# Optimization experiments

Hardware: AMD Instinct MI355X
Metric: run time of the kernel (lower is better)

The kernel has to match this reference:

```python
import jax, jax.numpy as jnp
import numpy as np

N_EMBD = 384
HEAD_SIZE = 64
B, T = 512, 256


def setup_inputs() -> dict:
    key = jax.random.key(0)
    ks = jax.random.split(key, 7)
    s = 1.0 / np.sqrt(N_EMBD)  # torch Linear default init scale
    return {
        "x": jax.random.normal(ks[0], (B, T, N_EMBD), dtype=jnp.float32),
        "Wq": jax.random.uniform(ks[1], (N_EMBD, HEAD_SIZE), jnp.float32, -s, s),
        "bq": jax.random.uniform(ks[2], (HEAD_SIZE,), jnp.float32, -s, s),
        "Wk": jax.random.uniform(ks[3], (N_EMBD, HEAD_SIZE), jnp.float32, -s, s),
        "bk": jax.random.uniform(ks[4], (HEAD_SIZE,), jnp.float32, -s, s),
        "Wv": jax.random.uniform(ks[5], (N_EMBD, HEAD_SIZE), jnp.float32, -s, s),
        "bv": jax.random.uniform(ks[6], (HEAD_SIZE,), jnp.float32, -s, s),
    }


def reference(x, Wq, bq, Wk, bk, Wv, bv):
    # Single causal self-attention head (nanoGPT 'Head', eval mode: dropout = identity)
    q = x @ Wq + bq  # [B, T, H]
    k = x @ Wk + bk
    v = x @ Wv + bv
    Tq = x.shape[1]
    scale = x.shape[-1] ** -0.5  # NOTE: source scales by n_embd (C), not head_size
    wei = jnp.einsum("btd,bsd->bts", q, k) * scale  # [B, T, T]
    mask = jnp.tril(jnp.ones((Tq, Tq), dtype=bool))
    wei = jnp.where(mask, wei, -jnp.inf)
    wei = jax.nn.softmax(wei, axis=-1)
    return jnp.einsum("bts,bsd->btd", wei, v)  # [B, T, H]
```

## Files before the change

### kernel.cpp

```cpp
#include <hip/hip_runtime.h>
#include <hip/hip_bf16.h>


#define Bsz 512
#define Tt  256
#define Cc  384
#define Hh  64

typedef __attribute__((ext_vector_type(8))) short bf16x8;
typedef __attribute__((ext_vector_type(4))) float f32x4;

__device__ __forceinline__ unsigned short f2bf(float f) {
    unsigned int u = __float_as_uint(f);
    unsigned int r = (u + 0x7fffu + ((u >> 16) & 1u)) >> 16;
    return (unsigned short)r;
}
__device__ __forceinline__ float bf2f(unsigned short b) {
    return __uint_as_float(((unsigned int)b) << 16);
}
__device__ __forceinline__ bf16x8 pack8(float4 a, float4 b) {
    union { __hip_bfloat162 h2[4]; bf16x8 v; } u;
    u.h2[0] = __float22bfloat162_rn(float2{a.x, a.y});
    u.h2[1] = __float22bfloat162_rn(float2{a.z, a.w});
    u.h2[2] = __float22bfloat162_rn(float2{b.x, b.y});
    u.h2[3] = __float22bfloat162_rn(float2{b.z, b.w});
    return u.v;
}
__device__ __forceinline__ void gload_lds16(const void* g, void* l) {
    __builtin_amdgcn_global_load_lds(
        (const __attribute__((address_space(1))) unsigned int*)g,
        (__attribute__((address_space(3))) unsigned int*)l, 16, 0, 0);
}

__global__ __launch_bounds__(256) void prep_kernel(const float* __restrict__ Wq,
                                                   const float* __restrict__ Wk,
                                                   const float* __restrict__ Wv,
                                                   unsigned short* __restrict__ wtf) {
    int idx = blockIdx.x * 256 + threadIdx.x;
    if (idx >= 192 * 384) return;
    int j = idx & 7;
    int l = (idx >> 3) & 63;
    int t = idx >> 9;
    int kc = t / 12, nt = t - kc * 12;
    int n = nt * 16 + (l & 15);
    int k = kc * 32 + (l >> 4) * 8 + j;
    const float* W = (n < 64) ? Wq : ((n < 128) ? Wk : Wv);
    wtf[idx] = f2bf(W[k * 64 + (n & 63)]);
}

__global__ __launch_bounds__(256, 2) void qkv_kernel(const float* __restrict__ x,
                                                     const float* __restrict__ bq,
                                                     const float* __restrict__ bk,
                                                     const float* __restrict__ bv,
                                                     const unsigned short* __restrict__ wtf,
                                                     unsigned short* __restrict__ qf,
                                                     unsigned short* __restrict__ kf,
                                                     unsigned short* __restrict__ vf) {
    __shared__ float xl[128 * 32];
    __shared__ unsigned short wtl[12 * 64 * 8];

    const int tid = threadIdx.x;
    const int w = tid >> 6, lane = tid & 63, quad = lane >> 4, cl = lane & 15;
    const int rb = blockIdx.x * 128;

    f32x4 acc[2][12];
#pragma unroll
    for (int rt = 0; rt < 2; ++rt)
#pragma unroll
        for (int nt = 0; nt < 12; ++nt) acc[rt][nt] = (f32x4){0.f, 0.f, 0.f, 0.f};

    for (int kc = 0; kc < 12; ++kc) {
#pragma unroll
        for (int i = 0; i < 4; ++i) {
            int s = i * 256 + tid;
            int row = s >> 3, cp = s & 7;
            int c = cp ^ (row & 7);
            gload_lds16(x + (size_t)(rb + row) * Cc + kc * 32 + c * 4,
                        (char*)xl + (size_t)s * 16);
        }
#pragma unroll
        for (int i = 0; i < 3; ++i) {
            int s = i * 256 + tid;
            gload_lds16(wtf + ((size_t)kc * 768 + s) * 8, (char*)wtl + (size_t)s * 16);
        }
        __syncthreads();

        bf16x8 a[2];
#pragma unroll
        for (int rt = 0; rt < 2; ++rt) {
            int R = w * 32 + rt * 16 + cl;
            float4 lo = *(const float4*)&xl[R * 32 + (((2 * quad) ^ (R & 7)) * 4)];
            float4 hi = *(const float4*)&xl[R * 32 + (((2 * quad + 1) ^ (R & 7)) * 4)];
            a[rt] = pack8(lo, hi);
        }
#pragma unroll
        for (int nt = 0; nt < 12; ++nt) {
            bf16x8 bfr = *(const bf16x8*)&wtl[(nt * 64 + lane) * 8];
            acc[0][nt] = __builtin_amdgcn_mfma_f32_16x16x32_bf16(a[0], bfr, acc[0][nt], 0, 0, 0);
            acc[1][nt] = __builtin_amdgcn_mfma_f32_16x16x32_bf16(a[1], bfr, acc[1][nt], 0, 0, 0);
        }
        __syncthreads();
    }

#pragma unroll
    for (int nt = 0; nt < 12; ++nt) {
        int col = nt * 16 + cl;
        if (col < 128) {
            float bias = (col < 64) ? bq[col] : bk[col - 64];
            unsigned short* dst = (col < 64) ? qf : kf;
            int h = col & 63;
            int sh = h >> 5, qp = (h >> 3) & 3, j = h & 7;
#pragma unroll
            for (int rt = 0; rt < 2; ++rt) {
                int m0 = rb + w * 32 + rt * 16 + quad * 4;
                size_t basei = (size_t)(m0 >> 4) * 1024 + sh * 512 + qp * 128 + quad * 32 + j;
#pragma unroll
                for (int r = 0; r < 4; ++r)
                    dst[basei + r * 8] = f2bf(acc[rt][nt][r] + bias);
            }
        } else {
            int h = col - 128;
            float bias = bv[h];
            int ht = h >> 4, clp = h & 15;
#pragma unroll
            for (int rt = 0; rt < 2; ++rt) {
                int m0 = rb + w * 32 + rt * 16 + quad * 4;
                int bI = m0 >> 8, t0 = m0 & 255;
                int ks2 = t0 >> 5, qp = (t0 >> 3) & 3, j0 = t0 & 7;
                unsigned long long pk =
                      (unsigned long long)f2bf(acc[rt][nt][0] + bias)
                    | ((unsigned long long)f2bf(acc[rt][nt][1] + bias) << 16)
                    | ((unsigned long long)f2bf(acc[rt][nt][2] + bias) << 32)
                    | ((unsigned long long)f2bf(acc[rt][nt][3] + bias) << 48);
                *(unsigned long long*)&vf[(size_t)((bI * 8 + ks2) * 4 + ht) * 512
                                          + qp * 128 + clp * 8 + j0] = pk;
            }
        }
    }
}

__global__ __launch_bounds__(256) void attn_kernel(const unsigned short* __restrict__ qf,
                                                   const unsigned short* __restrict__ kf,
                                                   const unsigned short* __restrict__ vf,
                                                   float* __restrict__ out) {
    __shared__ unsigned short Pl[4 * 512];

    const int tid = threadIdx.x;
    const int w = tid >> 6, lane = tid & 63, quad = lane >> 4, cl = lane & 15;
    const int b = blockIdx.y;
    const int W = blockIdx.x * 4 + w;
    const int qrow0 = W * 16;
    unsigned short* P = &Pl[w * 512];
    const float SL2E = 0.07362224f;

    const size_t gq = (size_t)(b * 16 + W) * 128;
    bf16x8 aq0 = *(const bf16x8*)&qf[(gq + lane) * 8];
    bf16x8 aq1 = *(const bf16x8*)&qf[(gq + 64 + lane) * 8];

    f32x4 o[4];
#pragma unroll
    for (int ht = 0; ht < 4; ++ht) o[ht] = (f32x4){0.f, 0.f, 0.f, 0.f};
    float rs[4] = {0.f, 0.f, 0.f, 0.f};

    const int nsteps = (qrow0 >> 5) + 1;
    for (int st = 0; st < nsteps; ++st) {
#pragma unroll
        for (int half = 0; half < 2; ++half) {
            int ct = st * 2 + half;
            size_t gk = (size_t)(b * 16 + ct) * 128;
            bf16x8 b0 = *(const bf16x8*)&kf[(gk + lane) * 8];
            bf16x8 b1 = *(const bf16x8*)&kf[(gk + 64 + lane) * 8];
            f32x4 sc = (f32x4){0.f, 0.f, 0.f, 0.f};
            sc = __builtin_amdgcn_mfma_f32_16x16x32_bf16(aq0, b0, sc, 0, 0, 0);
            sc = __builtin_amdgcn_mfma_f32_16x16x32_bf16(aq1, b1, sc, 0, 0, 0);
            int key = ct * 16 + cl;
#pragma unroll
            for (int r = 0; r < 4; ++r) {
                int row = quad * 4 + r;
                float p = (key <= qrow0 + row) ? exp2f(sc[r] * SL2E) : 0.f;
                unsigned short pb = f2bf(p);
                rs[r] += bf2f(pb);
                int k32 = half * 16 + cl;
                int chunk = (k32 >> 3) ^ quad;
                P[row * 32 + chunk * 8 + (k32 & 7)] = pb;
            }
        }
        bf16x8 bvf[4];
#pragma unroll
        for (int ht = 0; ht < 4; ++ht)
            bvf[ht] = *(const bf16x8*)&vf[((size_t)((b * 8 + st) * 4 + ht) * 64 + lane) * 8];

        asm volatile("s_waitcnt lgkmcnt(0)" ::: "memory");
        bf16x8 ap = *(const bf16x8*)((const char*)P + cl * 64 + ((quad ^ (cl >> 2)) & 3) * 16);
#pragma unroll
        for (int ht = 0; ht < 4; ++ht)
            o[ht] = __builtin_amdgcn_mfma_f32_16x16x32_bf16(ap, bvf[ht], o[ht], 0, 0, 0);
    }

#pragma unroll
    for (int r = 0; r < 4; ++r) {
        float s = rs[r];
        s += __shfl_xor(s, 1);
        s += __shfl_xor(s, 2);
        s += __shfl_xor(s, 4);
        s += __shfl_xor(s, 8);
        float inv = 1.0f / s;
        int t = qrow0 + quad * 4 + r;
#pragma unroll
        for (int ht = 0; ht < 4; ++ht)
            out[((size_t)(b * Tt + t)) * Hh + ht * 16 + cl] = o[ht][r] * inv;
    }
}

extern "C" void kernel_launch(void* const* d_in, const int* in_sizes, int n_in,
                              void* d_out, int out_size, void* d_ws, size_t ws_size,
                              hipStream_t stream) {
    const float* x  = (const float*)d_in[0];
    const float* Wq = (const float*)d_in[1];
    const float* bq = (const float*)d_in[2];
    const float* Wk = (const float*)d_in[3];
    const float* bk = (const float*)d_in[4];
    const float* Wv = (const float*)d_in[5];
    const float* bv = (const float*)d_in[6];
    float* out = (float*)d_out;

    char* ws = (char*)d_ws;
    unsigned short* wtf = (unsigned short*)(ws);
    unsigned short* qf  = (unsigned short*)(ws + (size_t)(1  << 20));
    unsigned short* kf  = (unsigned short*)(ws + (size_t)(17 << 20));
    unsigned short* vf  = (unsigned short*)(ws + (size_t)(33 << 20));

    prep_kernel<<<288, 256, 0, stream>>>(Wq, Wk, Wv, wtf);
    qkv_kernel<<<1024, 256, 0, stream>>>(x, bq, bk, bv, wtf, qf, kf, vf);
    attn_kernel<<<dim3(4, Bsz), 256, 0, stream>>>(qf, kf, vf, out);
}
```

Before: 338.3 us.

## Fuse QKV projection and causal attention into one per-batch kernel

Merges the QKV projection and attention kernels into one 512-thread block per batch element. Q, K and V stay in shared memory instead of going through global workspace. The x tiles are double-buffered with async LDS loads, and weight fragments are read straight from global into registers instead of being staged in LDS. The causal work is balanced by having each wave handle query tiles w and 15-w. The cost is large LDS use (about 114 KB) and only 512 blocks, which may limit occupancy and latency hiding.

```diff
diff --git a/kernel.cpp b/kernel.cpp
--- a/kernel.cpp
+++ b/kernel.cpp
@@ -48,20 +48,22 @@
     wtf[idx] = f2bf(W[k * 64 + (n & 63)]);
 }
 
-__global__ __launch_bounds__(256, 2) void qkv_kernel(const float* __restrict__ x,
-                                                     const float* __restrict__ bq,
-                                                     const float* __restrict__ bk,
-                                                     const float* __restrict__ bv,
-                                                     const unsigned short* __restrict__ wtf,
-                                                     unsigned short* __restrict__ qf,
-                                                     unsigned short* __restrict__ kf,
-                                                     unsigned short* __restrict__ vf) {
-    __shared__ float xl[128 * 32];
-    __shared__ unsigned short wtl[12 * 64 * 8];
+__global__ __launch_bounds__(512, 2) void fused_kernel(
+        const float* __restrict__ x,
+        const float* __restrict__ bq,
+        const float* __restrict__ bk,
+        const float* __restrict__ bv,
+        const unsigned short* __restrict__ wtf,
+        float* __restrict__ out) {
+    __shared__ float xl[2][256 * 32];
+    __shared__ unsigned short kl[16 * 128 * 8];
+    __shared__ unsigned short vl[8 * 4 * 64 * 8];
+    __shared__ unsigned short Pl[8 * 512];
 
     const int tid = threadIdx.x;
     const int w = tid >> 6, lane = tid & 63, quad = lane >> 4, cl = lane & 15;
-    const int rb = blockIdx.x * 128;
+    const int b = blockIdx.x;
+    const int rb = b * 256;
 
     f32x4 acc[2][12];
 #pragma unroll
@@ -69,54 +71,77 @@
 #pragma unroll
         for (int nt = 0; nt < 12; ++nt) acc[rt][nt] = (f32x4){0.f, 0.f, 0.f, 0.f};
 
+#pragma unroll
+    for (int i = 0; i < 4; ++i) {
+        int s = i * 512 + tid;
+        int row = s >> 3, cp = s & 7;
+        int c = cp ^ (row & 7);
+        gload_lds16(x + (size_t)(rb + row) * Cc + c * 4, (char*)xl[0] + (size_t)s * 16);
+    }
+
     for (int kc = 0; kc < 12; ++kc) {
-#pragma unroll
-        for (int i = 0; i < 4; ++i) {
-            int s = i * 256 + tid;
-            int row = s >> 3, cp = s & 7;
-            int c = cp ^ (row & 7);
-            gload_lds16(x + (size_t)(rb + row) * Cc + kc * 32 + c * 4,
-                        (char*)xl + (size_t)s * 16);
-        }
-#pragma unroll
-        for (int i = 0; i < 3; ++i) {
-            int s = i * 256 + tid;
-            gload_lds16(wtf + ((size_t)kc * 768 + s) * 8, (char*)wtl + (size_t)s * 16);
-        }
-        __syncthreads();
+        const int cur = kc & 1;
+        bf16x8 bfr[12];
+#pragma unroll
+        for (int nt = 0; nt < 12; ++nt)
+            bfr[nt] = *(const bf16x8*)&wtf[((size_t)(kc * 12 + nt) * 64 + lane) * 8];
+        if (kc < 11) {
+#pragma unroll
+            for (int i = 0; i < 4; ++i) {
+                int s = i * 512 + tid;
+                int row = s >> 3, cp = s & 7;
+                int c = cp ^ (row & 7);
+                gload_lds16(x + (size_t)(rb + row) * Cc + (kc + 1) * 32 + c * 4,
+                            (char*)xl[cur ^ 1] + (size_t)s * 16);
+            }
+            asm volatile("s_waitcnt vmcnt(4)" ::: "memory");
+        } else {
+            asm volatile("s_waitcnt vmcnt(0)" ::: "memory");
+        }
+        __builtin_amdgcn_s_barrier();
 
         bf16x8 a[2];
 #pragma unroll
         for (int rt = 0; rt < 2; ++rt) {
             int R = w * 32 + rt * 16 + cl;
-            float4 lo = *(const float4*)&xl[R * 32 + (((2 * quad) ^ (R & 7)) * 4)];
-            float4 hi = *(const float4*)&xl[R * 32 + (((2 * quad + 1) ^ (R & 7)) * 4)];
+            float4 lo = *(const float4*)&xl[cur][R * 32 + (((2 * quad) ^ (R & 7)) * 4)];
+            float4 hi = *(const float4*)&xl[cur][R * 32 + (((2 * quad + 1) ^ (R & 7)) * 4)];
             a[rt] = pack8(lo, hi);
         }
 #pragma unroll
         for (int nt = 0; nt < 12; ++nt) {
-            bf16x8 bfr = *(const bf16x8*)&wtl[(nt * 64 + lane) * 8];
-            acc[0][nt] = __builtin_amdgcn_mfma_f32_16x16x32_bf16(a[0], bfr, acc[0][nt], 0, 0, 0);
-            acc[1][nt] = __builtin_amdgcn_mfma_f32_16x16x32_bf16(a[1], bfr, acc[1][nt], 0, 0, 0);
-        }
-        __syncthreads();
-    }
-
+            acc[0][nt] = __builtin_amdgcn_mfma_f32_16x16x32_bf16(a[0], bfr[nt], acc[0][nt], 0, 0, 0);
+            acc[1][nt] = __builtin_amdgcn_mfma_f32_16x16x32_bf16(a[1], bfr[nt], acc[1][nt], 0, 0, 0);
+        }
+        __builtin_amdgcn_s_barrier();
+    }
+
+    unsigned short* qls = (unsigned short*)xl[0];
 #pragma unroll
     for (int nt = 0; nt < 12; ++nt) {
         int col = nt * 16 + cl;
-        if (col < 128) {
-            float bias = (col < 64) ? bq[col] : bk[col - 64];
-            unsigned short* dst = (col < 64) ? qf : kf;
+        if (nt < 4) {
+            float bias = bq[col];
+            int sh = col >> 5, qp = (col >> 3) & 3, j = col & 7;
+#pragma unroll
+            for (int rt = 0; rt < 2; ++rt) {
+                int m0 = w * 32 + rt * 16 + quad * 4;
+                int basei = (m0 >> 4) * 1024 + sh * 512 + qp * 128 + quad * 32 + j;
+#pragma unroll
+                for (int r = 0; r < 4; ++r)
+                    qls[basei + r * 8] = f2bf(acc[rt][nt][r] + bias);
+            }
+        } else if (nt < 8) {
             int h = col & 63;
+            float bias = bk[h];
             int sh = h >> 5, qp = (h >> 3) & 3, j = h & 7;
 #pragma unroll
             for (int rt = 0; rt < 2; ++rt) {
-                int m0 = rb + w * 32 + rt * 16 + quad * 4;
-                size_t basei = (size_t)(m0 >> 4) * 1024 + sh * 512 + qp * 128 + quad * 32 + j;
+                int m0 = w * 32 + rt * 16 + quad * 4;
+                int basei = (m0 >> 4) * 1024 + sh * 512 + qp * 128 + quad * 32 + j;
 #pragma unroll
                 for (int r = 0; r < 4; ++r)
-                    dst[basei + r * 8] = f2bf(acc[rt][nt][r] + bias);
+                    kl[basei + r * 8] = f2bf(acc[rt][nt][r] + bias);
             }
         } else {
             int h = col - 128;
@@ -124,91 +149,80 @@
             int ht = h >> 4, clp = h & 15;
 #pragma unroll
             for (int rt = 0; rt < 2; ++rt) {
-                int m0 = rb + w * 32 + rt * 16 + quad * 4;
-                int bI = m0 >> 8, t0 = m0 & 255;
-                int ks2 = t0 >> 5, qp = (t0 >> 3) & 3, j0 = t0 & 7;
+                int m0 = w * 32 + rt * 16 + quad * 4;
+                int ks2 = m0 >> 5, qp = (m0 >> 3) & 3, j0 = m0 & 7;
                 unsigned long long pk =
                       (unsigned long long)f2bf(acc[rt][nt][0] + bias)
                     | ((unsigned long long)f2bf(acc[rt][nt][1] + bias) << 16)
                     | ((unsigned long long)f2bf(acc[rt][nt][2] + bias) << 32)
                     | ((unsigned long long)f2bf(acc[rt][nt][3] + bias) << 48);
-                *(unsigned long long*)&vf[(size_t)((bI * 8 + ks2) * 4 + ht) * 512
-                                          + qp * 128 + clp * 8 + j0] = pk;
-            }
-        }
-    }
-}
-
-__global__ __launch_bounds__(256) void attn_kernel(const unsigned short* __restrict__ qf,
-                                                   const unsigned short* __restrict__ kf,
-                                                   const unsigned short* __restrict__ vf,
-                                                   float* __restrict__ out) {
-    __shared__ unsigned short Pl[4 * 512];
-
-    const int tid = threadIdx.x;
-    const int w = tid >> 6, lane = tid & 63, quad = lane >> 4, cl = lane & 15;
-    const int b = blockIdx.y;
-    const int W = blockIdx.x * 4 + w;
-    const int qrow0 = W * 16;
+                *(unsigned long long*)&vl[(ks2 * 4 + ht) * 512 + qp * 128 + clp * 8 + j0] = pk;
+            }
+        }
+    }
+    __syncthreads();
+
+    const float SL2E = 0.07362224f;
     unsigned short* P = &Pl[w * 512];
-    const float SL2E = 0.07362224f;
-
-    const size_t gq = (size_t)(b * 16 + W) * 128;
-    bf16x8 aq0 = *(const bf16x8*)&qf[(gq + lane) * 8];
-    bf16x8 aq1 = *(const bf16x8*)&qf[(gq + 64 + lane) * 8];
-
-    f32x4 o[4];
-#pragma unroll
-    for (int ht = 0; ht < 4; ++ht) o[ht] = (f32x4){0.f, 0.f, 0.f, 0.f};
-    float rs[4] = {0.f, 0.f, 0.f, 0.f};
-
-    const int nsteps = (qrow0 >> 5) + 1;
-    for (int st = 0; st < nsteps; ++st) {
-#pragma unroll
-        for (int half = 0; half < 2; ++half) {
-            int ct = st * 2 + half;
-            size_t gk = (size_t)(b * 16 + ct) * 128;
-            bf16x8 b0 = *(const bf16x8*)&kf[(gk + lane) * 8];
-            bf16x8 b1 = *(const bf16x8*)&kf[(gk + 64 + lane) * 8];
-            f32x4 sc = (f32x4){0.f, 0.f, 0.f, 0.f};
-            sc = __builtin_amdgcn_mfma_f32_16x16x32_bf16(aq0, b0, sc, 0, 0, 0);
-            sc = __builtin_amdgcn_mfma_f32_16x16x32_bf16(aq1, b1, sc, 0, 0, 0);
-            int key = ct * 16 + cl;
-#pragma unroll
-            for (int r = 0; r < 4; ++r) {
-                int row = quad * 4 + r;
-                float p = (key <= qrow0 + row) ? exp2f(sc[r] * SL2E) : 0.f;
-                unsigned short pb = f2bf(p);
-                rs[r] += bf2f(pb);
-                int k32 = half * 16 + cl;
-                int chunk = (k32 >> 3) ^ quad;
-                P[row * 32 + chunk * 8 + (k32 & 7)] = pb;
-            }
-        }
-        bf16x8 bvf[4];
-#pragma unroll
-        for (int ht = 0; ht < 4; ++ht)
-            bvf[ht] = *(const bf16x8*)&vf[((size_t)((b * 8 + st) * 4 + ht) * 64 + lane) * 8];
-
-        asm volatile("s_waitcnt lgkmcnt(0)" ::: "memory");
-        bf16x8 ap = *(const bf16x8*)((const char*)P + cl * 64 + ((quad ^ (cl >> 2)) & 3) * 16);
-#pragma unroll
-        for (int ht = 0; ht < 4; ++ht)
-            o[ht] = __builtin_amdgcn_mfma_f32_16x16x32_bf16(ap, bvf[ht], o[ht], 0, 0, 0);
-    }
-
-#pragma unroll
-    for (int r = 0; r < 4; ++r) {
-        float s = rs[r];
-        s += __shfl_xor(s, 1);
-        s += __shfl_xor(s, 2);
-        s += __shfl_xor(s, 4);
-        s += __shfl_xor(s, 8);
-        float inv = 1.0f / s;
-        int t = qrow0 + quad * 4 + r;
-#pragma unroll
-        for (int ht = 0; ht < 4; ++ht)
-            out[((size_t)(b * Tt + t)) * Hh + ht * 16 + cl] = o[ht][r] * inv;
+#pragma unroll
+    for (int ti = 0; ti < 2; ++ti) {
+        const int W = ti ? (15 - w) : w;
+        const int qrow0 = W * 16;
+        bf16x8 aq0 = *(const bf16x8*)&qls[(W * 128 + lane) * 8];
+        bf16x8 aq1 = *(const bf16x8*)&qls[(W * 128 + 64 + lane) * 8];
+
+        f32x4 o[4];
+#pragma unroll
+        for (int ht = 0; ht < 4; ++ht) o[ht] = (f32x4){0.f, 0.f, 0.f, 0.f};
+        float rs[4] = {0.f, 0.f, 0.f, 0.f};
+
+        const int nsteps = (qrow0 >> 5) + 1;
+        for (int st = 0; st < nsteps; ++st) {
+#pragma unroll
+            for (int half = 0; half < 2; ++half) {
+                int ct = st * 2 + half;
+                bf16x8 b0 = *(const bf16x8*)&kl[(ct * 128 + lane) * 8];
+                bf16x8 b1 = *(const bf16x8*)&kl[(ct * 128 + 64 + lane) * 8];
+                f32x4 sc = (f32x4){0.f, 0.f, 0.f, 0.f};
+                sc = __builtin_amdgcn_mfma_f32_16x16x32_bf16(aq0, b0, sc, 0, 0, 0);
+                sc = __builtin_amdgcn_mfma_f32_16x16x32_bf16(aq1, b1, sc, 0, 0, 0);
+                int key = ct * 16 + cl;
+#pragma unroll
+                for (int r = 0; r < 4; ++r) {
+                    int row = quad * 4 + r;
+                    float p = (key <= qrow0 + row) ? exp2f(sc[r] * SL2E) : 0.f;
+                    unsigned short pb = f2bf(p);
+                    rs[r] += bf2f(pb);
+                    int k32 = half * 16 + cl;
+                    int chunk = (k32 >> 3) ^ quad;
+                    P[row * 32 + chunk * 8 + (k32 & 7)] = pb;
+                }
+            }
+            bf16x8 bvf[4];
+#pragma unroll
+            for (int ht = 0; ht < 4; ++ht)
+                bvf[ht] = *(const bf16x8*)&vl[((st * 4 + ht) * 64 + lane) * 8];
+
+            asm volatile("s_waitcnt lgkmcnt(0)" ::: "memory");
+            bf16x8 ap = *(const bf16x8*)((const char*)P + cl * 64 + ((quad ^ (cl >> 2)) & 3) * 16);
+#pragma unroll
+            for (int ht = 0; ht < 4; ++ht)
+                o[ht] = __builtin_amdgcn_mfma_f32_16x16x32_bf16(ap, bvf[ht], o[ht], 0, 0, 0);
+        }
+
+#pragma unroll
+        for (int r = 0; r < 4; ++r) {
+            float s = rs[r];
+            s += __shfl_xor(s, 1);
+            s += __shfl_xor(s, 2);
+            s += __shfl_xor(s, 4);
+            s += __shfl_xor(s, 8);
+            float inv = 1.0f / s;
+            int t = qrow0 + quad * 4 + r;
+#pragma unroll
+            for (int ht = 0; ht < 4; ++ht)
+                out[((size_t)(b * Tt + t)) * Hh + ht * 16 + cl] = o[ht][r] * inv;
+        }
     }
 }
 
@@ -224,13 +238,8 @@
     const float* bv = (const float*)d_in[6];
     float* out = (float*)d_out;
 
-    char* ws = (char*)d_ws;
-    unsigned short* wtf = (unsigned short*)(ws);
-    unsigned short* qf  = (unsigned short*)(ws + (size_t)(1  << 20));
-    unsigned short* kf  = (unsigned short*)(ws + (size_t)(17 << 20));
-    unsigned short* vf  = (unsigned short*)(ws + (size_t)(33 << 20));
+    unsigned short* wtf = (unsigned short*)d_ws;
 
     prep_kernel<<<288, 256, 0, stream>>>(Wq, Wk, Wv, wtf);
-    qkv_kernel<<<1024, 256, 0, stream>>>(x, bq, bk, bv, wtf, qf, kf, vf);
-    attn_kernel<<<dim3(4, Bsz), 256, 0, stream>>>(qf, kf, vf, out);
-}
+    fused_kernel<<<Bsz, 512, 0, stream>>>(x, bq, bk, bv, wtf, out);
+}
```

New measurement: 320.8 us. 5.2% less time.

## Load x straight to registers and double-buffer weight tiles in the QKV kernel

Applied to the files above, without the earlier changes.

The QKV projection kernel no longer stages x through LDS. Each lane loads its own fp32 x fragment from global memory into registers and prefetches the next K-chunk while MFMAs run on the current one. Weight tiles are double-buffered in LDS, so each iteration needs one barrier instead of two, and the launch-bounds occupancy hint rises from 2 to 3 blocks per CU. This aims to overlap memory traffic for x and weights with compute. The cost is higher register pressure and per-lane global loads that may coalesce less well than the earlier LDS path.

```diff
diff --git a/kernel.cpp b/kernel.cpp
--- a/kernel.cpp
+++ b/kernel.cpp
@@ -18,12 +18,12 @@
 __device__ __forceinline__ float bf2f(unsigned short b) {
     return __uint_as_float(((unsigned int)b) << 16);
 }
-__device__ __forceinline__ bf16x8 pack8(float4 a, float4 b) {
+__device__ __forceinline__ bf16x8 pack8v(f32x4 a, f32x4 b) {
     union { __hip_bfloat162 h2[4]; bf16x8 v; } u;
-    u.h2[0] = __float22bfloat162_rn(float2{a.x, a.y});
-    u.h2[1] = __float22bfloat162_rn(float2{a.z, a.w});
-    u.h2[2] = __float22bfloat162_rn(float2{b.x, b.y});
-    u.h2[3] = __float22bfloat162_rn(float2{b.z, b.w});
+    u.h2[0] = __float22bfloat162_rn(float2{a[0], a[1]});
+    u.h2[1] = __float22bfloat162_rn(float2{a[2], a[3]});
+    u.h2[2] = __float22bfloat162_rn(float2{b[0], b[1]});
+    u.h2[3] = __float22bfloat162_rn(float2{b[2], b[3]});
     return u.v;
 }
 __device__ __forceinline__ void gload_lds16(const void* g, void* l) {
@@ -48,7 +48,7 @@
     wtf[idx] = f2bf(W[k * 64 + (n & 63)]);
 }
 
-__global__ __launch_bounds__(256, 2) void qkv_kernel(const float* __restrict__ x,
+__global__ __launch_bounds__(256, 3) void qkv_kernel(const float* __restrict__ x,
                                                      const float* __restrict__ bq,
                                                      const float* __restrict__ bk,
                                                      const float* __restrict__ bv,
@@ -56,8 +56,7 @@
                                                      unsigned short* __restrict__ qf,
                                                      unsigned short* __restrict__ kf,
                                                      unsigned short* __restrict__ vf) {
-    __shared__ float xl[128 * 32];
-    __shared__ unsigned short wtl[12 * 64 * 8];
+    __shared__ unsigned short wtl[2][6144];
 
     const int tid = threadIdx.x;
     const int w = tid >> 6, lane = tid & 63, quad = lane >> 4, cl = lane & 15;
@@ -69,37 +68,44 @@
 #pragma unroll
         for (int nt = 0; nt < 12; ++nt) acc[rt][nt] = (f32x4){0.f, 0.f, 0.f, 0.f};
 
-    for (int kc = 0; kc < 12; ++kc) {
-#pragma unroll
-        for (int i = 0; i < 4; ++i) {
-            int s = i * 256 + tid;
-            int row = s >> 3, cp = s & 7;
-            int c = cp ^ (row & 7);
-            gload_lds16(x + (size_t)(rb + row) * Cc + kc * 32 + c * 4,
-                        (char*)xl + (size_t)s * 16);
-        }
-#pragma unroll
-        for (int i = 0; i < 3; ++i) {
-            int s = i * 256 + tid;
-            gload_lds16(wtf + ((size_t)kc * 768 + s) * 8, (char*)wtl + (size_t)s * 16);
-        }
+#define STAGE_W(c_) {                                                                \
+    const unsigned short* s_ = wtf + (size_t)(c_) * 6144;                            \
+    unsigned short* d_ = &wtl[(c_) & 1][0];                                          \
+    gload_lds16(s_ + tid * 8, d_ + tid * 8);                                         \
+    gload_lds16(s_ + (256 + tid) * 8, d_ + (256 + tid) * 8);                         \
+    gload_lds16(s_ + (512 + tid) * 8, d_ + (512 + tid) * 8); }
+
+    const float* xp0 = x + ((size_t)rb + w * 32 + cl) * Cc + quad * 8;
+    const float* xp1 = xp0 + 16 * Cc;
+
+    f32x4 Xc0, Xc1, Xc2, Xc3, Xn0, Xn1, Xn2, Xn3;
+    STAGE_W(0);
+    Xc0 = *(const f32x4*)(xp0);
+    Xc1 = *(const f32x4*)(xp0 + 4);
+    Xc2 = *(const f32x4*)(xp1);
+    Xc3 = *(const f32x4*)(xp1 + 4);
+
+#pragma unroll 1
+    for (int k = 0; k < 12; ++k) {
         __syncthreads();
-
-        bf16x8 a[2];
-#pragma unroll
-        for (int rt = 0; rt < 2; ++rt) {
-            int R = w * 32 + rt * 16 + cl;
-            float4 lo = *(const float4*)&xl[R * 32 + (((2 * quad) ^ (R & 7)) * 4)];
-            float4 hi = *(const float4*)&xl[R * 32 + (((2 * quad + 1) ^ (R & 7)) * 4)];
-            a[rt] = pack8(lo, hi);
-        }
-#pragma unroll
-        for (int nt = 0; nt < 12; ++nt) {
-            bf16x8 bfr = *(const bf16x8*)&wtl[(nt * 64 + lane) * 8];
-            acc[0][nt] = __builtin_amdgcn_mfma_f32_16x16x32_bf16(a[0], bfr, acc[0][nt], 0, 0, 0);
-            acc[1][nt] = __builtin_amdgcn_mfma_f32_16x16x32_bf16(a[1], bfr, acc[1][nt], 0, 0, 0);
-        }
-        __syncthreads();
+        if (k < 11) {
+            STAGE_W(k + 1);
+            Xn0 = *(const f32x4*)(xp0 + (k + 1) * 32);
+            Xn1 = *(const f32x4*)(xp0 + (k + 1) * 32 + 4);
+            Xn2 = *(const f32x4*)(xp1 + (k + 1) * 32);
+            Xn3 = *(const f32x4*)(xp1 + (k + 1) * 32 + 4);
+        }
+        {
+            bf16x8 a0 = pack8v(Xc0, Xc1), a1 = pack8v(Xc2, Xc3);
+            const unsigned short* wb = &wtl[k & 1][0];
+#pragma unroll
+            for (int nt = 0; nt < 12; ++nt) {
+                bf16x8 bfr = *(const bf16x8*)&wb[(nt * 64 + lane) * 8];
+                acc[0][nt] = __builtin_amdgcn_mfma_f32_16x16x32_bf16(a0, bfr, acc[0][nt], 0, 0, 0);
+                acc[1][nt] = __builtin_amdgcn_mfma_f32_16x16x32_bf16(a1, bfr, acc[1][nt], 0, 0, 0);
+            }
+        }
+        Xc0 = Xn0; Xc1 = Xn1; Xc2 = Xn2; Xc3 = Xn3;
     }
 
 #pragma unroll
```

After: 343.7 us. Within noise of the previous version (+1.6%).
